# Kernel tuning notes

Measured on AMD Instinct MI355X. Metric: run time of the kernel, lower is better.

Reference implementation:

```python
import jax, jax.numpy as jnp
import numpy as np


def setup_inputs() -> dict:
    key = jax.random.key(0)
    ks = jax.random.split(key, 5)
    S, B, D, H, CTX = 2, 1024, 128, 512, 128
    W_SCALE = 0.05
    return {
        "context": jax.random.normal(ks[0], (B, CTX), dtype=jnp.float32),
        "eps": jax.random.normal(ks[1], (S, B, D), dtype=jnp.float32),
        "W1": jax.random.normal(ks[2], (H, D), dtype=jnp.float32) * W_SCALE,
        "Wc": jax.random.normal(ks[3], (H, CTX), dtype=jnp.float32) * W_SCALE,
        "b1": jnp.zeros((H,), dtype=jnp.float32),
        "W2": jax.random.normal(ks[4], (2 * D, H), dtype=jnp.float32) * W_SCALE,
        "b2": jnp.zeros((2 * D,), dtype=jnp.float32),
    }


def _made_masks(D, H, dtype):
    # standard MADE natural-ordering masks, 1 hidden layer, 2 output params per dim
    m_in = jnp.arange(1, D + 1)                      # input degrees 1..D
    m_h = (jnp.arange(H) % (D - 1)) + 1              # hidden degrees 1..D-1
    M1 = (m_h[:, None] >= m_in[None, :]).astype(dtype)   # (H, D)
    m_out = jnp.tile(m_in, 2)                        # (2D,) mean then pre_scale
    M2 = (m_out[:, None] > m_h[None, :]).astype(dtype)   # (2D, H)
    return M1, M2


def reference(context, eps, W1, Wc, b1, W2, b2):
    # for d in range(D): full MADE forward, take column d of (mu, scale),
    # z[:, d] = mu_d + softplus(pre_scale_d) * eps_d  (reparameterized Normal sample)
    S, B, D = eps.shape
    H = W1.shape[0]
    M1, M2 = _made_masks(D, H, W1.dtype)
    W1m = W1 * M1            # (H, D)
    W2m = W2 * M2            # (2D, H)
    ctx_term = context @ Wc.T + b1   # (B, H), shared across S samples

    def made(z):             # z: (S, B, D) -> (S, B, 2D)
        h = jax.nn.relu(jnp.einsum('sbd,hd->sbh', z, W1m) + ctx_term)
        return jnp.einsum('sbh,oh->sbo', h, W2m) + b2

    def step(z, xs):
        d, eps_d = xs        # d: scalar int, eps_d: (S, B)
        out = made(z)        # full re-forward each dim, as in the torch loop
        mu_d = jnp.take(out, d, axis=-1)             # (S, B)
        pre_scale_d = jnp.take(out, d + D, axis=-1)  # (S, B)
        scale_d = jax.nn.softplus(pre_scale_d)
        z_d = mu_d + scale_d * eps_d                 # Normal(mu, scale).rsample()
        z = z.at[:, :, d].set(z_d)                   # index_put on column d
        return z, None

    z0 = jnp.zeros_like(eps)
    xs = (jnp.arange(D), jnp.moveaxis(eps, -1, 0))   # per-step noise (D, S, B)
    z_samples, _ = jax.lax.scan(step, z0, xs)
    return z_samples
```

## Files before the change

kernel.cpp:

```cpp
#include <hip/hip_runtime.h>
#include <math.h>

constexpr int S_   = 2;
constexpr int B_   = 1024;
constexpr int D_   = 128;
constexpr int H_   = 512;
constexpr int CTX_ = 128;

__device__ __forceinline__ int h_of_u(int u) {
    return (u < 508) ? ((u >> 2) + 127 * (u & 3)) : u;
}
__device__ __forceinline__ int g_of_u(int u) {
    return (u < 508) ? ((u >> 2) + 1) : (u - 507);
}
__device__ __forceinline__ float rlaneF(float v, int l) {
    return __int_as_float(__builtin_amdgcn_readlane(__float_as_int(v), l));
}
__device__ __forceinline__ float softplus_fast(float x) {
    return __logf(1.f + __expf(x));
}

typedef unsigned int  uint32x4 __attribute__((ext_vector_type(4)));
typedef unsigned int  uint32x2 __attribute__((ext_vector_type(2)));
typedef _Float16      half8    __attribute__((ext_vector_type(8)));
typedef _Float16      half4v   __attribute__((ext_vector_type(4)));
typedef _Float16      half2v   __attribute__((ext_vector_type(2)));
typedef __fp16        fp16x2   __attribute__((ext_vector_type(2)));
union U16 { uint32x4 u; half8 h; half2v h2[4]; };
union U8  { uint32x2 u; half4v h; };
union H2U { half2v h; fp16x2 f; unsigned int u; };
union FU  { uint32x4 u; float4 f; };

#if __has_builtin(__builtin_amdgcn_fdot2)
__device__ __forceinline__ float fdot2f(half2v a, half2v b, float c) {
    return __builtin_amdgcn_fdot2(a, b, c, false);
}
#else
__device__ __forceinline__ float fdot2f(half2v a, half2v b, float c) {
    return fmaf((float)a[0], (float)b[0], fmaf((float)a[1], (float)b[1], c));
}
#endif
#if __has_builtin(__builtin_amdgcn_cvt_pkrtz)
__device__ __forceinline__ half2v pk2(float a, float b) {
    H2U t; t.f = __builtin_amdgcn_cvt_pkrtz(a, b);
    return t.h;
}
#else
__device__ __forceinline__ half2v pk2(float a, float b) {
    half2v r; r[0] = (_Float16)a; r[1] = (_Float16)b; return r;
}
#endif

constexpr int N_WT = 16 * 2048;
constexpr size_t WS_WT_OFF   = 0;
constexpr size_t WS_W0_OFF   = (size_t)N_WT * 16;
constexpr size_t WS_WPX_OFF  = WS_W0_OFF + 128 * 16;
constexpr size_t WS_CTXP_OFF = WS_WPX_OFF + 256 * 8;
constexpr size_t WS_NEED     = WS_CTXP_OFF + (size_t)B_ * H_ * 4;

__global__ __launch_bounds__(512) void prep10_kernel(
    const float* __restrict__ context, const float* __restrict__ Wc,
    const float* __restrict__ b1, const float* __restrict__ W1,
    const float* __restrict__ W2, float* __restrict__ ctxp,
    uint32x4* __restrict__ WT, float4* __restrict__ W0,
    uint32x2* __restrict__ Wpx)
{
    const int bid = (int)blockIdx.x;
    if (bid < 128) {
        const int b0 = bid * 8;
        const int u  = (int)threadIdx.x;
        const int h  = h_of_u(u);
        const float* wr = Wc + (size_t)h * CTX_;
        float bb = b1[h];
        float acc[8];
#pragma unroll
        for (int i = 0; i < 8; ++i) acc[i] = bb;
        for (int c = 0; c < CTX_; c += 4) {
            float4 wv4 = *reinterpret_cast<const float4*>(wr + c);
#pragma unroll
            for (int i = 0; i < 8; ++i) {
                const float* cr = context + (size_t)(b0 + i) * CTX_ + c;
                acc[i] = fmaf(wv4.x, cr[0], fmaf(wv4.y, cr[1],
                         fmaf(wv4.z, cr[2], fmaf(wv4.w, cr[3], acc[i]))));
            }
        }
#pragma unroll
        for (int i = 0; i < 8; ++i)
            ctxp[(size_t)(b0 + i) * H_ + u] = acc[i];
        return;
    }
    if (bid < 192) {
        int e = (bid - 128) * 512 + (int)threadIdx.x;
        int m = e >> 11, r = e & 2047, t = r >> 8, k = (r >> 6) & 3, L = r & 63;
        int d = 8 * m + 1 + t;
        uint32x4 o = (uint32x4){0u, 0u, 0u, 0u};
        if (d <= 127) {
            int p = (d - 1) >> 4;
            if (k <= 1) {
                U16 uu;
                int rowA = (k == 0) ? L : (64 + L);
                int rowB = (k == 0) ? (128 + L) : (192 + L);
#pragma unroll
                for (int i = 0; i < 4; ++i) {
                    int hu = h_of_u(4 * (d - 1) + i);
                    uu.h[i]     = (_Float16)W2[(size_t)rowA * H_ + hu];
                    uu.h[4 + i] = (_Float16)W2[(size_t)rowB * H_ + hu];
                }
                o = uu.u;
            } else {
                FU f;
                int qb = (k == 2) ? 0 : 4;
#pragma unroll
                for (int q = 0; q < 4; ++q) {
                    int s = qb + q + p;
                    float val = 0.f;
                    if (s < 8) {
                        int u_ = s * 64 + L;
                        if (g_of_u(u_) > d) val = W1[(size_t)h_of_u(u_) * D_ + d];
                    }
                    ((float*)&f.f)[q] = val;
                }
                o = f.u;
            }
        }
        WT[e] = o;
        return;
    }
    int i = (int)threadIdx.x;
    if (i < 128) {
        int L = i & 63, qb = (i >> 6) * 4;
        float4 f;
        float* fp = (float*)&f;
#pragma unroll
        for (int q = 0; q < 4; ++q) {
            int u_ = (qb + q) * 64 + L;
            fp[q] = W1[(size_t)h_of_u(u_) * D_ + 0];
        }
        W0[i] = f;
    } else if (i < 384) {
        int k = i - 128, t = k >> 6, L = k & 63, u_ = 508 + t;
        U8 o;
        o.h[0] = (_Float16)W2[(size_t)L * H_ + u_];
        o.h[1] = (_Float16)W2[(size_t)(128 + L) * H_ + u_];
        o.h[2] = (_Float16)W2[(size_t)(64 + L) * H_ + u_];
        o.h[3] = (_Float16)W2[(size_t)(192 + L) * H_ + u_];
        Wpx[k] = o.u;
    }
}

#define LOFF(HALF, T, K) ((HALF) * 2048 + (T) * 256 + (K) * 64)

#define STEP_LO(HALF, T, DB, LASTT, EXTRA) do {                               \
    U16 wA_, wB_;                                                             \
    wA_.u = smL[LOFF(HALF, T, 0)];                                            \
    wB_.u = smL[LOFF(HALF, T, 1)];                                            \
    const float4 wu0_ = *(const float4*)&smL[LOFF(HALF, T, 2)];               \
    const float4 wu1_ = *(const float4*)&smL[LOFF(HALF, T, 3)];               \
    float v_ = fmaxf(a0, 0.f);                                                \
    half2v s01_ = pk2(rlaneF(v_, 32 * (HALF) + 4 * (T) + 0),                  \
                      rlaneF(v_, 32 * (HALF) + 4 * (T) + 1));                 \
    half2v s23_ = pk2(rlaneF(v_, 32 * (HALF) + 4 * (T) + 2),                  \
                      rlaneF(v_, 32 * (HALF) + 4 * (T) + 3));                 \
    acc0 = fdot2f(wA_.h2[0], s01_, acc0);                                     \
    acc0 = fdot2f(wA_.h2[1], s23_, acc0);                                     \
    acc1 = fdot2f(wA_.h2[2], s01_, acc1);                                     \
    acc1 = fdot2f(wA_.h2[3], s23_, acc1);                                     \
    acc2 = fdot2f(wB_.h2[0], s01_, acc2);                                     \
    acc2 = fdot2f(wB_.h2[1], s23_, acc2);                                     \
    acc3 = fdot2f(wB_.h2[2], s01_, acc3);                                     \
    acc3 = fdot2f(wB_.h2[3], s23_, acc3);                                     \
    EXTRA                                                                     \
    const int dl_ = (DB) + (T);                                               \
    const bool hi64_ = (LASTT);                                               \
    float mu_ = hi64_ ? acc2 : acc0;                                          \
    float pv_ = hi64_ ? acc3 : acc1;                                          \
    float e_  = hi64_ ? rlaneF(eH, 0) : rlaneF(eL, dl_ & 63);                 \
    float z_  = fmaf(softplus_fast(pv_), e_, mu_);                            \
    float zb_ = rlaneF(z_, dl_ & 63);                                         \
    zlo = (!hi64_ && L == dl_) ? zb_ : zlo;                                   \
    zhi = (hi64_ && L == 0)    ? zb_ : zhi;                                   \
    a0 = fmaf(wu0_.x, zb_, a0); a1 = fmaf(wu0_.y, zb_, a1);                   \
    a2 = fmaf(wu0_.z, zb_, a2); a3 = fmaf(wu0_.w, zb_, a3);                   \
    a4 = fmaf(wu1_.x, zb_, a4); a5 = fmaf(wu1_.y, zb_, a5);                   \
    a6 = fmaf(wu1_.z, zb_, a6); a7 = fmaf(wu1_.w, zb_, a7);                   \
} while (0)

#define STEP_HI(HALF, T, DB2) do {                                            \
    U16 wB_;                                                                  \
    wB_.u = smL[LOFF(HALF, T, 1)];                                            \
    const float4 wu_ = *(const float4*)&smL[LOFF(HALF, T, 2)];                \
    float v_ = fmaxf(a0, 0.f);                                                \
    half2v s01_ = pk2(rlaneF(v_, 32 * (HALF) + 4 * (T) + 0),                  \
                      rlaneF(v_, 32 * (HALF) + 4 * (T) + 1));                 \
    half2v s23_ = pk2(rlaneF(v_, 32 * (HALF) + 4 * (T) + 2),                  \
                      rlaneF(v_, 32 * (HALF) + 4 * (T) + 3));                 \
    acc2 = fdot2f(wB_.h2[0], s01_, acc2);                                     \
    acc2 = fdot2f(wB_.h2[1], s23_, acc2);                                     \
    acc3 = fdot2f(wB_.h2[2], s01_, acc3);                                     \
    acc3 = fdot2f(wB_.h2[3], s23_, acc3);                                     \
    const int dl_ = (DB2) + (T);                                              \
    float e_  = rlaneF(eH, dl_ & 63);                                         \
    float z_  = fmaf(softplus_fast(acc3), e_, acc2);                          \
    float zb_ = rlaneF(z_, dl_ & 63);                                         \
    zhi = (L == dl_) ? zb_ : zhi;                                             \
    a0 = fmaf(wu_.x, zb_, a0); a1 = fmaf(wu_.y, zb_, a1);                     \
    a2 = fmaf(wu_.z, zb_, a2); a3 = fmaf(wu_.w, zb_, a3);                     \
} while (0)

#define EXTRA_X(T, WXn) {                                                     \
    float v7_ = fmaxf(a7, 0.f);                                               \
    float sx_ = rlaneF(v7_, 60 + (T));                                        \
    acc0 = fmaf((float)WXn.h[0], sx_, acc0);                                  \
    acc1 = fmaf((float)WXn.h[1], sx_, acc1);                                  \
    acc2 = fmaf((float)WXn.h[2], sx_, acc2);                                  \
    acc3 = fmaf((float)WXn.h[3], sx_, acc3); }

#define ROTATE do { a0=a1; a1=a2; a2=a3; a3=a4; a4=a5; a5=a6; a6=a7; } while (0)

#define STAGE_LO_X(m) { x0 = WT[(m)*2048 + tid];        x1 = WT[(m)*2048 + 512 + tid];  \
                        x2 = WT[(m)*2048 + 1024 + tid]; x3 = WT[(m)*2048 + 1536 + tid]; }
#define STAGE_LO_Y(m) { y0 = WT[(m)*2048 + tid];        y1 = WT[(m)*2048 + 512 + tid];  \
                        y2 = WT[(m)*2048 + 1024 + tid]; y3 = WT[(m)*2048 + 1536 + tid]; }
#define STAGE_HI_X(m) { x0 = WT[(m)*2048 + ehi]; x1 = WT[(m)*2048 + 1024 + ehi]; }
#define STAGE_HI_Y(m) { y0 = WT[(m)*2048 + ehi]; y1 = WT[(m)*2048 + 1024 + ehi]; }
#define COMMIT_LO_X(BB) { sm[(BB)+tid] = x0; sm[(BB)+512+tid] = x1;                     \
                          sm[(BB)+1024+tid] = x2; sm[(BB)+1536+tid] = x3; }
#define COMMIT_LO_Y(BB) { sm[(BB)+tid] = y0; sm[(BB)+512+tid] = y1;                     \
                          sm[(BB)+1024+tid] = y2; sm[(BB)+1536+tid] = y3; }
#define COMMIT_HI_X(BB) { sm[(BB)+ehi] = x0; sm[(BB)+1024+ehi] = x1; }
#define COMMIT_HI_Y(BB) { sm[(BB)+ehi] = y0; sm[(BB)+1024+ehi] = y1; }

__global__ __launch_bounds__(512) void ar10_kernel(
    const float* __restrict__ eps, const uint32x4* __restrict__ WT,
    const float4* __restrict__ W0, const uint32x2* __restrict__ Wpx2,
    const float* __restrict__ b2, const float* __restrict__ ctxp,
    float* __restrict__ out)
{
    __shared__ uint32x4 sm[4096];
    const int tid = (int)threadIdx.x;
    const int w   = tid >> 6, L = tid & 63;
    const int wv  = (int)blockIdx.x * 8 + w;
    const int b   = wv & (B_ - 1);
    const uint32x4* smL = sm + L;
    const int ehi = ((tid >> 7) << 8) + 64 + (tid & 127);

    uint32x4 x0, x1, x2, x3, y0, y1, y2, y3;
    STAGE_LO_X(0);

    float a0 = ctxp[(size_t)b * H_ + 0 * 64 + L];
    float a1 = ctxp[(size_t)b * H_ + 1 * 64 + L];
    float a2 = ctxp[(size_t)b * H_ + 2 * 64 + L];
    float a3 = ctxp[(size_t)b * H_ + 3 * 64 + L];
    float a4 = ctxp[(size_t)b * H_ + 4 * 64 + L];
    float a5 = ctxp[(size_t)b * H_ + 5 * 64 + L];
    float a6 = ctxp[(size_t)b * H_ + 6 * 64 + L];
    float a7 = ctxp[(size_t)b * H_ + 7 * 64 + L];
    float acc0 = b2[L],      acc1 = b2[128 + L];
    float acc2 = b2[64 + L], acc3 = b2[192 + L];
    const float* ep = eps + (size_t)wv * D_;
    float eL = ep[L], eH = ep[64 + L];
    float zlo = 0.f, zhi = 0.f;
    float4 w0lo = W0[L], w0hi = W0[64 + L];
    U8 wx1, wx2, wx3, wx4;
    wx1.u = Wpx2[0 * 64 + L]; wx2.u = Wpx2[1 * 64 + L];
    wx3.u = Wpx2[2 * 64 + L]; wx4.u = Wpx2[3 * 64 + L];

    COMMIT_LO_X(0);
    STAGE_LO_Y(1);

    {
        float e_ = rlaneF(eL, 0);
        float z_ = fmaf(softplus_fast(acc1), e_, acc0);
        float zb = rlaneF(z_, 0);
        zlo = (L == 0) ? zb : zlo;
        a0 = fmaf(w0lo.x, zb, a0); a1 = fmaf(w0lo.y, zb, a1);
        a2 = fmaf(w0lo.z, zb, a2); a3 = fmaf(w0lo.w, zb, a3);
        a4 = fmaf(w0hi.x, zb, a4); a5 = fmaf(w0hi.y, zb, a5);
        a6 = fmaf(w0hi.z, zb, a6); a7 = fmaf(w0hi.w, zb, a7);
    }
    __syncthreads();

    {
        STEP_LO(0, 0, 1, false, EXTRA_X(0, wx1));
        STEP_LO(0, 1, 1, false, EXTRA_X(1, wx2));
        STEP_LO(0, 2, 1, false, EXTRA_X(2, wx3));
        STEP_LO(0, 3, 1, false, EXTRA_X(3, wx4));
        STEP_LO(0, 4, 1, false, {});
        STEP_LO(0, 5, 1, false, {});
        STEP_LO(0, 6, 1, false, {});
        STEP_LO(0, 7, 1, false, {});
        COMMIT_LO_Y(2048);
        STAGE_LO_X(2);
        __syncthreads();
    }
    {
        STEP_LO(1, 0, 9, false, {});
        STEP_LO(1, 1, 9, false, {});
        STEP_LO(1, 2, 9, false, {});
        STEP_LO(1, 3, 9, false, {});
        STEP_LO(1, 4, 9, false, {});
        STEP_LO(1, 5, 9, false, {});
        STEP_LO(1, 6, 9, false, {});
        STEP_LO(1, 7, 9, false, {});
        COMMIT_LO_X(0);
        STAGE_LO_Y(3);
        ROTATE;
        __syncthreads();
    }

#pragma unroll 1
    for (int mm = 1; mm <= 3; ++mm) {
        const int dbE = 16 * mm + 1, dbO = dbE + 8;
        const bool last = (mm == 3);
        STEP_LO(0, 0, dbE, false, {});
        STEP_LO(0, 1, dbE, false, {});
        STEP_LO(0, 2, dbE, false, {});
        STEP_LO(0, 3, dbE, false, {});
        STEP_LO(0, 4, dbE, false, {});
        STEP_LO(0, 5, dbE, false, {});
        STEP_LO(0, 6, dbE, false, {});
        STEP_LO(0, 7, dbE, false, {});
        COMMIT_LO_Y(2048);
        if (!last) { STAGE_LO_X(2 * mm + 2); } else { STAGE_HI_X(8); }
        __syncthreads();
        STEP_LO(1, 0, dbO, false, {});
        STEP_LO(1, 1, dbO, false, {});
        STEP_LO(1, 2, dbO, false, {});
        STEP_LO(1, 3, dbO, false, {});
        STEP_LO(1, 4, dbO, false, {});
        STEP_LO(1, 5, dbO, false, {});
        STEP_LO(1, 6, dbO, false, {});
        STEP_LO(1, 7, dbO, last, {});
        if (!last) { COMMIT_LO_X(0); } else { COMMIT_HI_X(0); }
        if (!last) { STAGE_LO_Y(2 * mm + 3); } else { STAGE_HI_Y(9); }
        ROTATE;
        __syncthreads();
    }

#pragma unroll 1
    for (int mm = 0; mm <= 3; ++mm) {
        const int dbE = 16 * mm + 1, dbO = dbE + 8;
        STEP_HI(0, 0, dbE);
        STEP_HI(0, 1, dbE);
        STEP_HI(0, 2, dbE);
        STEP_HI(0, 3, dbE);
        STEP_HI(0, 4, dbE);
        STEP_HI(0, 5, dbE);
        STEP_HI(0, 6, dbE);
        STEP_HI(0, 7, dbE);
        COMMIT_HI_Y(2048);
        if (mm < 3) { STAGE_HI_X(10 + 2 * mm); }
        __syncthreads();
        STEP_HI(1, 0, dbO);
        STEP_HI(1, 1, dbO);
        STEP_HI(1, 2, dbO);
        STEP_HI(1, 3, dbO);
        STEP_HI(1, 4, dbO);
        STEP_HI(1, 5, dbO);
        STEP_HI(1, 6, dbO);
        STEP_HI(1, 7, dbO);
        if (mm < 3) {
            COMMIT_HI_X(0);
            STAGE_HI_Y(11 + 2 * mm);
            ROTATE;
            __syncthreads();
        }
    }

    out[(size_t)wv * D_ + L]      = zlo;
    out[(size_t)wv * D_ + 64 + L] = zhi;
}

template <int CTRL>
__device__ __forceinline__ float dpp_add(float x)
{
    int r = __builtin_amdgcn_update_dpp(0, __float_as_int(x), CTRL, 0xF, 0xF, true);
    return x + __int_as_float(r);
}
__device__ __forceinline__ float reduce64(float x)
{
    x = dpp_add<0x111>(x);
    x = dpp_add<0x112>(x);
    x = dpp_add<0x114>(x);
    x = dpp_add<0x118>(x);
    x = dpp_add<0x142>(x);
    x = dpp_add<0x143>(x);
    return __int_as_float(__builtin_amdgcn_readlane(__float_as_int(x), 63));
}
__device__ __forceinline__ float softplus_safe(float x) {
    return fmaxf(x, 0.f) + __logf(1.f + __expf(-fabsf(x)));
}

__global__ __launch_bounds__(256) void ar_fallback_kernel(
    const float* __restrict__ eps,
    const float* __restrict__ W2,
    const float* __restrict__ b2,
    const float* __restrict__ context,
    const float* __restrict__ Wc,
    const float* __restrict__ b1,
    const float* __restrict__ W1,
    float* __restrict__ out)
{
    const int wave = (int)((blockIdx.x * blockDim.x + threadIdx.x) >> 6);
    const int lane = (int)(threadIdx.x & 63);
    if (wave >= S_ * B_) return;
    const int b  = wave % B_;
    const int hb = lane * 8;

    int mh[8];
#pragma unroll
    for (int j = 0; j < 8; ++j) mh[j] = ((hb + j) % (D_ - 1)) + 1;

    float a[8];
#pragma unroll
    for (int j = 0; j < 8; ++j) a[j] = b1[hb + j];
    for (int c = 0; c < CTX_; ++c) {
        float cv = context[(size_t)b * CTX_ + c];
#pragma unroll
        for (int j = 0; j < 8; ++j)
            a[j] = fmaf(Wc[(size_t)(hb + j) * CTX_ + c], cv, a[j]);
    }

    const float* epsrow = eps + (size_t)wave * D_;
    float* outrow = out + (size_t)wave * D_;
    float zr0 = 0.f, zr1 = 0.f;

    for (int d = 0; d < D_; ++d) {
        const float* w2mu = W2 + (size_t)d * H_ + hb;
        const float* w2ps = W2 + (size_t)(d + D_) * H_ + hb;
        float4 m0 = *reinterpret_cast<const float4*>(w2mu);
        float4 m1 = *reinterpret_cast<const float4*>(w2mu + 4);
        float4 p0 = *reinterpret_cast<const float4*>(w2ps);
        float4 p1 = *reinterpret_cast<const float4*>(w2ps + 4);
        float wmu[8] = {m0.x, m0.y, m0.z, m0.w, m1.x, m1.y, m1.z, m1.w};
        float wps[8] = {p0.x, p0.y, p0.z, p0.w, p1.x, p1.y, p1.z, p1.w};
        float w1v[8];
#pragma unroll
        for (int j = 0; j < 8; ++j) w1v[j] = W1[(size_t)(hb + j) * D_ + d];
        float eps_d = epsrow[d];

        float mu = 0.f, ps = 0.f;
#pragma unroll
        for (int j = 0; j < 8; ++j) {
            float r = fmaxf(a[j], 0.f);
            r = (mh[j] <= d) ? r : 0.f;
            mu = fmaf(wmu[j], r, mu);
            ps = fmaf(wps[j], r, ps);
        }
        mu = reduce64(mu) + b2[d];
        ps = reduce64(ps) + b2[d + D_];

        float z = fmaf(softplus_safe(ps), eps_d, mu);
#pragma unroll
        for (int j = 0; j < 8; ++j) {
            float wgt = (mh[j] <= d) ? 0.f : w1v[j];
            a[j] = fmaf(wgt, z, a[j]);
        }
        bool mine = (lane == (d & 63));
        if (d < 64) zr0 = mine ? z : zr0; else zr1 = mine ? z : zr1;
    }

    outrow[lane]      = zr0;
    outrow[lane + 64] = zr1;
}

extern "C" void kernel_launch(void* const* d_in, const int* in_sizes, int n_in,
                              void* d_out, int out_size, void* d_ws, size_t ws_size,
                              hipStream_t stream)
{
    const float* context = (const float*)d_in[0];
    const float* eps     = (const float*)d_in[1];
    const float* W1      = (const float*)d_in[2];
    const float* Wc      = (const float*)d_in[3];
    const float* b1      = (const float*)d_in[4];
    const float* W2      = (const float*)d_in[5];
    const float* b2      = (const float*)d_in[6];
    float* out = (float*)d_out;

    if (ws_size >= WS_NEED) {
        char* ws = (char*)d_ws;
        uint32x4* WT   = (uint32x4*)(ws + WS_WT_OFF);
        float4*   W0   = (float4*)(ws + WS_W0_OFF);
        uint32x2* Wpx  = (uint32x2*)(ws + WS_WPX_OFF);
        float*    ctxp = (float*)(ws + WS_CTXP_OFF);

        prep10_kernel<<<193, 512, 0, stream>>>(
            context, Wc, b1, W1, W2, ctxp, WT, W0, Wpx);

        ar10_kernel<<<256, 512, 0, stream>>>(
            eps, WT, W0, Wpx, b2, ctxp, out);
    } else {
        const int nwaves = S_ * B_;
        ar_fallback_kernel<<<(nwaves * 64) / 256, 256, 0, stream>>>(
            eps, W2, b2, context, Wc, b1, W1, out);
    }
}
```

Measured before the change: 45.76 us.

## Pack W1 update weights as fp16 and software-pipeline LDS weight reads

The per-step W1 update weights move from fp32 float4 pairs to packed fp16 (one 16-byte entry instead of two), which shrinks the weight table, LDS footprint and per-stage global staging from four entries per thread to three. The high-half phase gets its own compact layout with 8-byte update entries and fewer staging threads. Shared-memory reads for the next step are issued one step ahead in double registers, so LDS latency overlaps the serial recursion. This trades some precision in the z-update weights (fp16 instead of fp32) and extra register pressure.

```diff
diff --git a/kernel.cpp b/kernel.cpp
--- a/kernel.cpp
+++ b/kernel.cpp
@@ -27,9 +27,8 @@
 typedef _Float16      half2v   __attribute__((ext_vector_type(2)));
 typedef __fp16        fp16x2   __attribute__((ext_vector_type(2)));
 union U16 { uint32x4 u; half8 h; half2v h2[4]; };
-union U8  { uint32x2 u; half4v h; };
+union U8  { uint32x2 u; half4v h; half2v h2[2]; };
 union H2U { half2v h; fp16x2 f; unsigned int u; };
-union FU  { uint32x4 u; float4 f; };
 
 #if __has_builtin(__builtin_amdgcn_fdot2)
 __device__ __forceinline__ float fdot2f(half2v a, half2v b, float c) {
@@ -51,14 +50,14 @@
 }
 #endif
 
-constexpr int N_WT = 16 * 2048;
 constexpr size_t WS_WT_OFF   = 0;
-constexpr size_t WS_W0_OFF   = (size_t)N_WT * 16;
+constexpr size_t WS_W0_OFF   = (size_t)16 * 1536 * 16;
 constexpr size_t WS_WPX_OFF  = WS_W0_OFF + 128 * 16;
 constexpr size_t WS_CTXP_OFF = WS_WPX_OFF + 256 * 8;
 constexpr size_t WS_NEED     = WS_CTXP_OFF + (size_t)B_ * H_ * 4;
-
-__global__ __launch_bounds__(512) void prep10_kernel(
+constexpr int N_WT_ENT = 8 * 1536 + 8 * 768;
+
+__global__ __launch_bounds__(512) void prep13_kernel(
     const float* __restrict__ context, const float* __restrict__ Wc,
     const float* __restrict__ b1, const float* __restrict__ W1,
     const float* __restrict__ W2, float* __restrict__ ctxp,
@@ -89,41 +88,79 @@
             ctxp[(size_t)(b0 + i) * H_ + u] = acc[i];
         return;
     }
-    if (bid < 192) {
+    if (bid < 164) {
         int e = (bid - 128) * 512 + (int)threadIdx.x;
-        int m = e >> 11, r = e & 2047, t = r >> 8, k = (r >> 6) & 3, L = r & 63;
-        int d = 8 * m + 1 + t;
-        uint32x4 o = (uint32x4){0u, 0u, 0u, 0u};
-        if (d <= 127) {
-            int p = (d - 1) >> 4;
+        if (e >= N_WT_ENT) return;
+        if (e < 12288) {
+            int m = e / 1536, r = e % 1536;
+            int t = r / 192, rr = r % 192, k = rr >> 6, L = rr & 63;
+            int d = 8 * m + 1 + t;
+            U16 o;
             if (k <= 1) {
-                U16 uu;
                 int rowA = (k == 0) ? L : (64 + L);
                 int rowB = (k == 0) ? (128 + L) : (192 + L);
 #pragma unroll
                 for (int i = 0; i < 4; ++i) {
                     int hu = h_of_u(4 * (d - 1) + i);
-                    uu.h[i]     = (_Float16)W2[(size_t)rowA * H_ + hu];
-                    uu.h[4 + i] = (_Float16)W2[(size_t)rowB * H_ + hu];
+                    o.h[i]     = (_Float16)W2[(size_t)rowA * H_ + hu];
+                    o.h[4 + i] = (_Float16)W2[(size_t)rowB * H_ + hu];
                 }
-                o = uu.u;
             } else {
-                FU f;
-                int qb = (k == 2) ? 0 : 4;
-#pragma unroll
-                for (int q = 0; q < 4; ++q) {
-                    int s = qb + q + p;
-                    float val = 0.f;
+                int p = (d - 1) >> 4;
+#pragma unroll
+                for (int j = 0; j < 8; ++j) {
+                    int s = j + p;
+                    _Float16 val = (_Float16)0.f;
                     if (s < 8) {
                         int u_ = s * 64 + L;
-                        if (g_of_u(u_) > d) val = W1[(size_t)h_of_u(u_) * D_ + d];
+                        if (g_of_u(u_) > d)
+                            val = (_Float16)W1[(size_t)h_of_u(u_) * D_ + d];
                     }
-                    ((float*)&f.f)[q] = val;
+                    o.h[j] = val;
                 }
-                o = f.u;
+            }
+            WT[e] = o.u;
+        } else {
+            int e2 = e - 12288;
+            int m = 8 + e2 / 768, r = e2 % 768;
+            int dbb = 8 * m + 1;
+            if (r < 512) {
+                int t = r >> 6, L = r & 63, d = dbb + t;
+                U16 o;
+#pragma unroll
+                for (int i = 0; i < 8; ++i) o.h[i] = (_Float16)0.f;
+                if (d <= 127) {
+#pragma unroll
+                    for (int i = 0; i < 4; ++i) {
+                        int hu = h_of_u(4 * (d - 1) + i);
+                        o.h[i]     = (_Float16)W2[(size_t)(64 + L) * H_ + hu];
+                        o.h[4 + i] = (_Float16)W2[(size_t)(192 + L) * H_ + hu];
+                    }
+                }
+                WT[(size_t)m * 1536 + t * 64 + L] = o.u;
+            } else {
+                int q = r - 512, t = q >> 5, j = q & 31, d = dbb + t;
+                int L0 = 2 * j, L1 = 2 * j + 1;
+                U8 oa, ob;
+                oa.u = (uint32x2){0u, 0u}; ob.u = (uint32x2){0u, 0u};
+                if (d <= 127) {
+                    int p = (d - 1) >> 4;
+#pragma unroll
+                    for (int k2 = 0; k2 < 4; ++k2) {
+                        int s = p + k2;
+                        _Float16 va = (_Float16)0.f, vb = (_Float16)0.f;
+                        if (s < 8) {
+                            int u0 = s * 64 + L0, u1 = s * 64 + L1;
+                            if (g_of_u(u0) > d) va = (_Float16)W1[(size_t)h_of_u(u0) * D_ + d];
+                            if (g_of_u(u1) > d) vb = (_Float16)W1[(size_t)h_of_u(u1) * D_ + d];
+                        }
+                        oa.h[k2] = va; ob.h[k2] = vb;
+                    }
+                }
+                uint32x4 o4 = (uint32x4){oa.u[0], oa.u[1], ob.u[0], ob.u[1]};
+                WT[(size_t)m * 1536 + 512 + q] = o4;
             }
         }
-        WT[e] = o;
         return;
     }
     int i = (int)threadIdx.x;
@@ -148,66 +185,69 @@
     }
 }
 
-#define LOFF(HALF, T, K) ((HALF) * 2048 + (T) * 256 + (K) * 64)
-
-#define STEP_LO(HALF, T, DB, LASTT, EXTRA) do {                               \
-    U16 wA_, wB_;                                                             \
-    wA_.u = smL[LOFF(HALF, T, 0)];                                            \
-    wB_.u = smL[LOFF(HALF, T, 1)];                                            \
-    const float4 wu0_ = *(const float4*)&smL[LOFF(HALF, T, 2)];               \
-    const float4 wu1_ = *(const float4*)&smL[LOFF(HALF, T, 3)];               \
+#define LOFF(HALF, T, K) ((HALF) * 1536 + (T) * 192 + (K) * 64)
+#define HOFF(HALF, T)    ((HALF) * 1536 + (T) * 64)
+#define HUOFF(HALF, T)   ((HALF) * 3072 + 1024 + (T) * 64)
+
+#define RDLO(HALF, T, RA, RB, RU) { RA.u = smL[LOFF(HALF, T, 0)];             \
+    RB.u = smL[LOFF(HALF, T, 1)]; RU.u = smL[LOFF(HALF, T, 2)]; }
+#define RDHI(HALF, T, RB, RU) { RB.u = smL[HOFF(HALF, T)];                    \
+    RU.u = smH2L[HUOFF(HALF, T)]; }
+
+#define SLO1(RA, RB, RU, DD, LASTT, EXTRA) do {                               \
+    const int d_ = (DD);                                                      \
+    const int lb_ = ((d_ - 1) & 15) << 2;                                     \
     float v_ = fmaxf(a0, 0.f);                                                \
-    half2v s01_ = pk2(rlaneF(v_, 32 * (HALF) + 4 * (T) + 0),                  \
-                      rlaneF(v_, 32 * (HALF) + 4 * (T) + 1));                 \
-    half2v s23_ = pk2(rlaneF(v_, 32 * (HALF) + 4 * (T) + 2),                  \
-                      rlaneF(v_, 32 * (HALF) + 4 * (T) + 3));                 \
-    acc0 = fdot2f(wA_.h2[0], s01_, acc0);                                     \
-    acc0 = fdot2f(wA_.h2[1], s23_, acc0);                                     \
-    acc1 = fdot2f(wA_.h2[2], s01_, acc1);                                     \
-    acc1 = fdot2f(wA_.h2[3], s23_, acc1);                                     \
-    acc2 = fdot2f(wB_.h2[0], s01_, acc2);                                     \
-    acc2 = fdot2f(wB_.h2[1], s23_, acc2);                                     \
-    acc3 = fdot2f(wB_.h2[2], s01_, acc3);                                     \
-    acc3 = fdot2f(wB_.h2[3], s23_, acc3);                                     \
+    half2v s01_ = pk2(rlaneF(v_, lb_ + 0), rlaneF(v_, lb_ + 1));              \
+    half2v s23_ = pk2(rlaneF(v_, lb_ + 2), rlaneF(v_, lb_ + 3));              \
+    acc0 = fdot2f(RA.h2[0], s01_, acc0);                                      \
+    acc0 = fdot2f(RA.h2[1], s23_, acc0);                                      \
+    acc1 = fdot2f(RA.h2[2], s01_, acc1);                                      \
+    acc1 = fdot2f(RA.h2[3], s23_, acc1);                                      \
+    acc2 = fdot2f(RB.h2[0], s01_, acc2);                                      \
+    acc2 = fdot2f(RB.h2[1], s23_, acc2);                                      \
+    acc3 = fdot2f(RB.h2[2], s01_, acc3);                                      \
+    acc3 = fdot2f(RB.h2[3], s23_, acc3);                                      \
     EXTRA                                                                     \
-    const int dl_ = (DB) + (T);                                               \
     const bool hi64_ = (LASTT);                                               \
     float mu_ = hi64_ ? acc2 : acc0;                                          \
     float pv_ = hi64_ ? acc3 : acc1;                                          \
-    float e_  = hi64_ ? rlaneF(eH, 0) : rlaneF(eL, dl_ & 63);                 \
+    float e_  = hi64_ ? rlaneF(eH, 0) : rlaneF(eL, d_ & 63);                  \
     float z_  = fmaf(softplus_fast(pv_), e_, mu_);                            \
-    float zb_ = rlaneF(z_, dl_ & 63);                                         \
-    zlo = (!hi64_ && L == dl_) ? zb_ : zlo;                                   \
-    zhi = (hi64_ && L == 0)    ? zb_ : zhi;                                   \
-    a0 = fmaf(wu0_.x, zb_, a0); a1 = fmaf(wu0_.y, zb_, a1);                   \
-    a2 = fmaf(wu0_.z, zb_, a2); a3 = fmaf(wu0_.w, zb_, a3);                   \
-    a4 = fmaf(wu1_.x, zb_, a4); a5 = fmaf(wu1_.y, zb_, a5);                   \
-    a6 = fmaf(wu1_.z, zb_, a6); a7 = fmaf(wu1_.w, zb_, a7);                   \
+    float zb_ = rlaneF(z_, d_ & 63);                                          \
+    zlo = (!hi64_ && L == d_) ? zb_ : zlo;                                    \
+    zhi = (hi64_ && L == 0)   ? zb_ : zhi;                                    \
+    a0 = fmaf((float)RU.h[0], zb_, a0);                                       \
+    a1 = fmaf((float)RU.h[1], zb_, a1);                                       \
+    a2 = fmaf((float)RU.h[2], zb_, a2);                                       \
+    a3 = fmaf((float)RU.h[3], zb_, a3);                                       \
+    a4 = fmaf((float)RU.h[4], zb_, a4);                                       \
+    a5 = fmaf((float)RU.h[5], zb_, a5);                                       \
+    a6 = fmaf((float)RU.h[6], zb_, a6);                                       \
+    a7 = fmaf((float)RU.h[7], zb_, a7);                                       \
 } while (0)
 
-#define STEP_HI(HALF, T, DB2) do {                                            \
-    U16 wB_;                                                                  \
-    wB_.u = smL[LOFF(HALF, T, 1)];                                            \
-    const float4 wu_ = *(const float4*)&smL[LOFF(HALF, T, 2)];                \
+#define SHI1(RB, RU, DL2) do {                                                \
+    const int d2_ = (DL2);                                                    \
+    const int lb_ = ((d2_ - 1) & 15) << 2;                                    \
     float v_ = fmaxf(a0, 0.f);                                                \
-    half2v s01_ = pk2(rlaneF(v_, 32 * (HALF) + 4 * (T) + 0),                  \
-                      rlaneF(v_, 32 * (HALF) + 4 * (T) + 1));                 \
-    half2v s23_ = pk2(rlaneF(v_, 32 * (HALF) + 4 * (T) + 2),                  \
-                      rlaneF(v_, 32 * (HALF) + 4 * (T) + 3));                 \
-    acc2 = fdot2f(wB_.h2[0], s01_, acc2);                                     \
-    acc2 = fdot2f(wB_.h2[1], s23_, acc2);                                     \
-    acc3 = fdot2f(wB_.h2[2], s01_, acc3);                                     \
-    acc3 = fdot2f(wB_.h2[3], s23_, acc3);                                     \
-    const int dl_ = (DB2) + (T);                                              \
-    float e_  = rlaneF(eH, dl_ & 63);                                         \
+    half2v s01_ = pk2(rlaneF(v_, lb_ + 0), rlaneF(v_, lb_ + 1));              \
+    half2v s23_ = pk2(rlaneF(v_, lb_ + 2), rlaneF(v_, lb_ + 3));              \
+    acc2 = fdot2f(RB.h2[0], s01_, acc2);                                      \
+    acc2 = fdot2f(RB.h2[1], s23_, acc2);                                      \
+    acc3 = fdot2f(RB.h2[2], s01_, acc3);                                      \
+    acc3 = fdot2f(RB.h2[3], s23_, acc3);                                      \
+    float e_  = rlaneF(eH, d2_ & 63);                                         \
     float z_  = fmaf(softplus_fast(acc3), e_, acc2);                          \
-    float zb_ = rlaneF(z_, dl_ & 63);                                         \
-    zhi = (L == dl_) ? zb_ : zhi;                                             \
-    a0 = fmaf(wu_.x, zb_, a0); a1 = fmaf(wu_.y, zb_, a1);                     \
-    a2 = fmaf(wu_.z, zb_, a2); a3 = fmaf(wu_.w, zb_, a3);                     \
+    float zb_ = rlaneF(z_, d2_ & 63);                                         \
+    zhi = (L == d2_) ? zb_ : zhi;                                             \
+    a0 = fmaf((float)RU.h[0], zb_, a0);                                       \
+    a1 = fmaf((float)RU.h[1], zb_, a1);                                       \
+    a2 = fmaf((float)RU.h[2], zb_, a2);                                       \
+    a3 = fmaf((float)RU.h[3], zb_, a3);                                       \
 } while (0)
 
-#define EXTRA_X(T, WXn) {                                                     \
+#define EXTRA_X1(T, WXn) {                                                    \
     float v7_ = fmaxf(a7, 0.f);                                               \
     float sx_ = rlaneF(v7_, 60 + (T));                                        \
     acc0 = fmaf((float)WXn.h[0], sx_, acc0);                                  \
@@ -215,36 +255,40 @@
     acc2 = fmaf((float)WXn.h[2], sx_, acc2);                                  \
     acc3 = fmaf((float)WXn.h[3], sx_, acc3); }
 
-#define ROTATE do { a0=a1; a1=a2; a2=a3; a3=a4; a4=a5; a5=a6; a6=a7; } while (0)
-
-#define STAGE_LO_X(m) { x0 = WT[(m)*2048 + tid];        x1 = WT[(m)*2048 + 512 + tid];  \
-                        x2 = WT[(m)*2048 + 1024 + tid]; x3 = WT[(m)*2048 + 1536 + tid]; }
-#define STAGE_LO_Y(m) { y0 = WT[(m)*2048 + tid];        y1 = WT[(m)*2048 + 512 + tid];  \
-                        y2 = WT[(m)*2048 + 1024 + tid]; y3 = WT[(m)*2048 + 1536 + tid]; }
-#define STAGE_HI_X(m) { x0 = WT[(m)*2048 + ehi]; x1 = WT[(m)*2048 + 1024 + ehi]; }
-#define STAGE_HI_Y(m) { y0 = WT[(m)*2048 + ehi]; y1 = WT[(m)*2048 + 1024 + ehi]; }
-#define COMMIT_LO_X(BB) { sm[(BB)+tid] = x0; sm[(BB)+512+tid] = x1;                     \
-                          sm[(BB)+1024+tid] = x2; sm[(BB)+1536+tid] = x3; }
-#define COMMIT_LO_Y(BB) { sm[(BB)+tid] = y0; sm[(BB)+512+tid] = y1;                     \
-                          sm[(BB)+1024+tid] = y2; sm[(BB)+1536+tid] = y3; }
-#define COMMIT_HI_X(BB) { sm[(BB)+ehi] = x0; sm[(BB)+1024+ehi] = x1; }
-#define COMMIT_HI_Y(BB) { sm[(BB)+ehi] = y0; sm[(BB)+1024+ehi] = y1; }
-
-__global__ __launch_bounds__(512) void ar10_kernel(
+#define ROT1 do { a0=a1; a1=a2; a2=a3; a3=a4; a4=a5; a5=a6; a6=a7; } while (0)
+
+#define STAGE_LO_X(m) { x0=WT[(m)*1536+tid]; x1=WT[(m)*1536+512+tid];         \
+    x2=WT[(m)*1536+1024+tid]; }
+#define STAGE_LO_Y(m) { y0=WT[(m)*1536+tid]; y1=WT[(m)*1536+512+tid];         \
+    y2=WT[(m)*1536+1024+tid]; }
+#define STAGE_HI_X(m) { x0=WT[(m)*1536+tid];                                  \
+    if (tid < 256) x1=WT[(m)*1536+512+tid]; }
+#define STAGE_HI_Y(m) { y0=WT[(m)*1536+tid];                                  \
+    if (tid < 256) y1=WT[(m)*1536+512+tid]; }
+#define COMMIT_LO_X(BB) { sm[(BB)+tid]=x0; sm[(BB)+512+tid]=x1;               \
+    sm[(BB)+1024+tid]=x2; }
+#define COMMIT_LO_Y(BB) { sm[(BB)+tid]=y0; sm[(BB)+512+tid]=y1;               \
+    sm[(BB)+1024+tid]=y2; }
+#define COMMIT_HI_X(BB) { sm[(BB)+tid]=x0;                                    \
+    if (tid < 256) sm[(BB)+512+tid]=x1; }
+#define COMMIT_HI_Y(BB) { sm[(BB)+tid]=y0;                                    \
+    if (tid < 256) sm[(BB)+512+tid]=y1; }
+
+__global__ __launch_bounds__(512) void ar13_kernel(
     const float* __restrict__ eps, const uint32x4* __restrict__ WT,
     const float4* __restrict__ W0, const uint32x2* __restrict__ Wpx2,
     const float* __restrict__ b2, const float* __restrict__ ctxp,
     float* __restrict__ out)
 {
-    __shared__ uint32x4 sm[4096];
+    __shared__ uint32x4 sm[3072];
     const int tid = (int)threadIdx.x;
     const int w   = tid >> 6, L = tid & 63;
     const int wv  = (int)blockIdx.x * 8 + w;
     const int b   = wv & (B_ - 1);
     const uint32x4* smL = sm + L;
-    const int ehi = ((tid >> 7) << 8) + 64 + (tid & 127);
-
-    uint32x4 x0, x1, x2, x3, y0, y1, y2, y3;
+    const uint32x2* smH2L = ((const uint32x2*)sm) + L;
+
+    uint32x4 x0, x1, x2, y0, y1, y2;
     STAGE_LO_X(0);
 
     float a0 = ctxp[(size_t)b * H_ + 0 * 64 + L];
@@ -261,9 +305,9 @@
     float eL = ep[L], eH = ep[64 + L];
     float zlo = 0.f, zhi = 0.f;
     float4 w0lo = W0[L], w0hi = W0[64 + L];
-    U8 wx1, wx2, wx3, wx4;
-    wx1.u = Wpx2[0 * 64 + L]; wx2.u = Wpx2[1 * 64 + L];
-    wx3.u = Wpx2[2 * 64 + L]; wx4.u = Wpx2[3 * 64 + L];
+    U8 wxa, wxb, wxc, wxd;
+    wxa.u = Wpx2[L];       wxb.u = Wpx2[64 + L];
+    wxc.u = Wpx2[128 + L]; wxd.u = Wpx2[192 + L];
 
     COMMIT_LO_X(0);
     STAGE_LO_Y(1);
@@ -280,89 +324,104 @@
     }
     __syncthreads();
 
+    U16 rA0, rB0, rU0, rA1, rB1, rU1;
+    U8  rU0h, rU1h;
+
     {
-        STEP_LO(0, 0, 1, false, EXTRA_X(0, wx1));
-        STEP_LO(0, 1, 1, false, EXTRA_X(1, wx2));
-        STEP_LO(0, 2, 1, false, EXTRA_X(2, wx3));
-        STEP_LO(0, 3, 1, false, EXTRA_X(3, wx4));
-        STEP_LO(0, 4, 1, false, {});
-        STEP_LO(0, 5, 1, false, {});
-        STEP_LO(0, 6, 1, false, {});
-        STEP_LO(0, 7, 1, false, {});
-        COMMIT_LO_Y(2048);
+        RDLO(0, 0, rA0, rB0, rU0);
+        RDLO(0, 1, rA1, rB1, rU1);
+        SLO1(rA0, rB0, rU0, 1, false, EXTRA_X1(0, wxa)); RDLO(0, 2, rA0, rB0, rU0);
+        SLO1(rA1, rB1, rU1, 2, false, EXTRA_X1(1, wxb)); RDLO(0, 3, rA1, rB1, rU1);
+        SLO1(rA0, rB0, rU0, 3, false, EXTRA_X1(2, wxc)); RDLO(0, 4, rA0, rB0, rU0);
+        SLO1(rA1, rB1, rU1, 4, false, EXTRA_X1(3, wxd)); RDLO(0, 5, rA1, rB1, rU1);
+        SLO1(rA0, rB0, rU0, 5, false, {});               RDLO(0, 6, rA0, rB0, rU0);
+        SLO1(rA1, rB1, rU1, 6, false, {});               RDLO(0, 7, rA1, rB1, rU1);
+        SLO1(rA0, rB0, rU0, 7, false, {});
+        SLO1(rA1, rB1, rU1, 8, false, {});
+        COMMIT_LO_Y(1536);
         STAGE_LO_X(2);
         __syncthreads();
     }
     {
-        STEP_LO(1, 0, 9, false, {});
-        STEP_LO(1, 1, 9, false, {});
-        STEP_LO(1, 2, 9, false, {});
-        STEP_LO(1, 3, 9, false, {});
-        STEP_LO(1, 4, 9, false, {});
-        STEP_LO(1, 5, 9, false, {});
-        STEP_LO(1, 6, 9, false, {});
-        STEP_LO(1, 7, 9, false, {});
+        RDLO(1, 0, rA0, rB0, rU0);
+        RDLO(1, 1, rA1, rB1, rU1);
+        SLO1(rA0, rB0, rU0,  9, false, {}); RDLO(1, 2, rA0, rB0, rU0);
+        SLO1(rA1, rB1, rU1, 10, false, {}); RDLO(1, 3, rA1, rB1, rU1);
+        SLO1(rA0, rB0, rU0, 11, false, {}); RDLO(1, 4, rA0, rB0, rU0);
+        SLO1(rA1, rB1, rU1, 12, false, {}); RDLO(1, 5, rA1, rB1, rU1);
+        SLO1(rA0, rB0, rU0, 13, false, {}); RDLO(1, 6, rA0, rB0, rU0);
+        SLO1(rA1, rB1, rU1, 14, false, {}); RDLO(1, 7, rA1, rB1, rU1);
+        SLO1(rA0, rB0, rU0, 15, false, {});
+        SLO1(rA1, rB1, rU1, 16, false, {});
         COMMIT_LO_X(0);
         STAGE_LO_Y(3);
-        ROTATE;
+        ROT1;
         __syncthreads();
     }
 
 #pragma unroll 1
     for (int mm = 1; mm <= 3; ++mm) {
-        const int dbE = 16 * mm + 1, dbO = dbE + 8;
+        const int dbE = 16 * mm, dbO = dbE + 8;
         const bool last = (mm == 3);
-        STEP_LO(0, 0, dbE, false, {});
-        STEP_LO(0, 1, dbE, false, {});
-        STEP_LO(0, 2, dbE, false, {});
-        STEP_LO(0, 3, dbE, false, {});
-        STEP_LO(0, 4, dbE, false, {});
-        STEP_LO(0, 5, dbE, false, {});
-        STEP_LO(0, 6, dbE, false, {});
-        STEP_LO(0, 7, dbE, false, {});
-        COMMIT_LO_Y(2048);
+        RDLO(0, 0, rA0, rB0, rU0);
+        RDLO(0, 1, rA1, rB1, rU1);
+        SLO1(rA0, rB0, rU0, dbE + 1, false, {}); RDLO(0, 2, rA0, rB0, rU0);
+        SLO1(rA1, rB1, rU1, dbE + 2, false, {}); RDLO(0, 3, rA1, rB1, rU1);
+        SLO1(rA0, rB0, rU0, dbE + 3, false, {}); RDLO(0, 4, rA0, rB0, rU0);
+        SLO1(rA1, rB1, rU1, dbE + 4, false, {}); RDLO(0, 5, rA1, rB1, rU1);
+        SLO1(rA0, rB0, rU0, dbE + 5, false, {}); RDLO(0, 6, rA0, rB0, rU0);
+        SLO1(rA1, rB1, rU1, dbE + 6, false, {}); RDLO(0, 7, rA1, rB1, rU1);
+        SLO1(rA0, rB0, rU0, dbE + 7, false, {});
+        SLO1(rA1, rB1, rU1, dbE + 8, false, {});
+        COMMIT_LO_Y(1536);
         if (!last) { STAGE_LO_X(2 * mm + 2); } else { STAGE_HI_X(8); }
         __syncthreads();
-        STEP_LO(1, 0, dbO, false, {});
-        STEP_LO(1, 1, dbO, false, {});
-        STEP_LO(1, 2, dbO, false, {});
-        STEP_LO(1, 3, dbO, false, {});
-        STEP_LO(1, 4, dbO, false, {});
-        STEP_LO(1, 5, dbO, false, {});
-        STEP_LO(1, 6, dbO, false, {});
-        STEP_LO(1, 7, dbO, last, {});
+        RDLO(1, 0, rA0, rB0, rU0);
+        RDLO(1, 1, rA1, rB1, rU1);
+        SLO1(rA0, rB0, rU0, dbO + 1, false, {}); RDLO(1, 2, rA0, rB0, rU0);
+        SLO1(rA1, rB1, rU1, dbO + 2, false, {}); RDLO(1, 3, rA1, rB1, rU1);
+        SLO1(rA0, rB0, rU0, dbO + 3, false, {}); RDLO(1, 4, rA0, rB0, rU0);
+        SLO1(rA1, rB1, rU1, dbO + 4, false, {}); RDLO(1, 5, rA1, rB1, rU1);
+        SLO1(rA0, rB0, rU0, dbO + 5, false, {}); RDLO(1, 6, rA0, rB0, rU0);
+        SLO1(rA1, rB1, rU1, dbO + 6, false, {}); RDLO(1, 7, rA1, rB1, rU1);
+        SLO1(rA0, rB0, rU0, dbO + 7, false, {});
+        SLO1(rA1, rB1, rU1, dbO + 8, last, {});
         if (!last) { COMMIT_LO_X(0); } else { COMMIT_HI_X(0); }
         if (!last) { STAGE_LO_Y(2 * mm + 3); } else { STAGE_HI_Y(9); }
-        ROTATE;
+        ROT1;
         __syncthreads();
     }
 
 #pragma unroll 1
     for (int mm = 0; mm <= 3; ++mm) {
-        const int dbE = 16 * mm + 1, dbO = dbE + 8;
-        STEP_HI(0, 0, dbE);
-        STEP_HI(0, 1, dbE);
-        STEP_HI(0, 2, dbE);
-        STEP_HI(0, 3, dbE);
-        STEP_HI(0, 4, dbE);
-        STEP_HI(0, 5, dbE);
-        STEP_HI(0, 6, dbE);
-        STEP_HI(0, 7, dbE);
-        COMMIT_HI_Y(2048);
+        const int dbE = 16 * mm, dbO = dbE + 8;
+        RDHI(0, 0, rB0, rU0h);
+        RDHI(0, 1, rB1, rU1h);
+        SHI1(rB0, rU0h, dbE + 1); RDHI(0, 2, rB0, rU0h);
+        SHI1(rB1, rU1h, dbE + 2); RDHI(0, 3, rB1, rU1h);
+        SHI1(rB0, rU0h, dbE + 3); RDHI(0, 4, rB0, rU0h);
+        SHI1(rB1, rU1h, dbE + 4); RDHI(0, 5, rB1, rU1h);
+        SHI1(rB0, rU0h, dbE + 5); RDHI(0, 6, rB0, rU0h);
+        SHI1(rB1, rU1h, dbE + 6); RDHI(0, 7, rB1, rU1h);
+        SHI1(rB0, rU0h, dbE + 7);
+        SHI1(rB1, rU1h, dbE + 8);
+        COMMIT_HI_Y(1536);
         if (mm < 3) { STAGE_HI_X(10 + 2 * mm); }
         __syncthreads();
-        STEP_HI(1, 0, dbO);
-        STEP_HI(1, 1, dbO);
-        STEP_HI(1, 2, dbO);
-        STEP_HI(1, 3, dbO);
-        STEP_HI(1, 4, dbO);
-        STEP_HI(1, 5, dbO);
-        STEP_HI(1, 6, dbO);
-        STEP_HI(1, 7, dbO);
+        RDHI(1, 0, rB0, rU0h);
+        RDHI(1, 1, rB1, rU1h);
+        SHI1(rB0, rU0h, dbO + 1); RDHI(1, 2, rB0, rU0h);
+        SHI1(rB1, rU1h, dbO + 2); RDHI(1, 3, rB1, rU1h);
+        SHI1(rB0, rU0h, dbO + 3); RDHI(1, 4, rB0, rU0h);
+        SHI1(rB1, rU1h, dbO + 4); RDHI(1, 5, rB1, rU1h);
+        SHI1(rB0, rU0h, dbO + 5); RDHI(1, 6, rB0, rU0h);
+        SHI1(rB1, rU1h, dbO + 6); RDHI(1, 7, rB1, rU1h);
+        SHI1(rB0, rU0h, dbO + 7);
+        SHI1(rB1, rU1h, dbO + 8);
         if (mm < 3) {
             COMMIT_HI_X(0);
             STAGE_HI_Y(11 + 2 * mm);
-            ROTATE;
+            ROT1;
             __syncthreads();
         }
     }
@@ -484,10 +543,10 @@
         uint32x2* Wpx  = (uint32x2*)(ws + WS_WPX_OFF);
         float*    ctxp = (float*)(ws + WS_CTXP_OFF);
 
-        prep10_kernel<<<193, 512, 0, stream>>>(
+        prep13_kernel<<<165, 512, 0, stream>>>(
             context, Wc, b1, W1, W2, ctxp, WT, W0, Wpx);
 
-        ar10_kernel<<<256, 512, 0, stream>>>(
+        ar13_kernel<<<256, 512, 0, stream>>>(
             eps, WT, W0, Wpx, b2, ctxp, out);
     } else {
         const int nwaves = S_ * B_;
```

New measurement: 42.94 us. -6.2%, faster.
